# Optimization experiments

Hardware: AMD Instinct MI355X
Metric: run time of the kernel (lower is better)

The kernel has to match this reference:

```python
import jax, jax.numpy as jnp
import numpy as np

C = 256          # channels
G = 16           # dcn groups
K = 3            # dcn kernel size (P = K*K sampling points)
PAD = 1
DIL = 1
OFFSET_SCALE = 1.0
HIDDEN = 4 * C   # mlp_ratio = 4
EPS = 1e-6


def layer_norm(x, g, b):
    mu = x.mean(-1, keepdims=True)
    var = jnp.mean((x - mu) ** 2, -1, keepdims=True)
    return (x - mu) * jax.lax.rsqrt(var + EPS) * g + b


def grid_sample_bilinear(img, grid):
    """img: (B,Cg,H,W); grid: (B,L,P,2) xy in [-1,1].
    Matches F.grid_sample(mode='bilinear', padding_mode='zeros', align_corners=False)."""
    B, Cg, H, W = img.shape
    x = (grid[..., 0] + 1.0) * (W * 0.5) - 0.5
    y = (grid[..., 1] + 1.0) * (H * 0.5) - 0.5
    x0f = jnp.floor(x); y0f = jnp.floor(y)
    wx1 = x - x0f; wy1 = y - y0f
    x0 = x0f.astype(jnp.int32); y0 = y0f.astype(jnp.int32)
    flat = img.reshape(B, Cg, H * W)

    def tap(ix, iy, w):
        valid = (ix >= 0) & (ix < W) & (iy >= 0) & (iy < H)
        idx = jnp.clip(iy, 0, H - 1) * W + jnp.clip(ix, 0, W - 1)
        v = jnp.take_along_axis(flat, idx.reshape(B, 1, -1), axis=2)
        v = v.reshape(B, Cg, idx.shape[1], idx.shape[2])
        return v * (w * valid)[:, None]

    return (tap(x0, y0, (1 - wx1) * (1 - wy1))
            + tap(x0 + 1, y0, wx1 * (1 - wy1))
            + tap(x0, y0 + 1, (1 - wx1) * wy1)
            + tap(x0 + 1, y0 + 1, wx1 * wy1))


def dcnv3(x, dw_w, dw_b, off_w, off_b, mask_w, mask_b, inp_w, inp_b, out_w, out_b):
    """DCNv3 forward (dcnv3_core_pytorch math), x: (N,H,W,C) channels_last."""
    N, H, W, Cc = x.shape
    Cg = Cc // G
    P = K * K
    xp = x @ inp_w.T + inp_b                             # input_proj
    x1 = jax.lax.conv_general_dilated(
        x, dw_w, (1, 1), [(PAD, PAD), (PAD, PAD)],
        dimension_numbers=('NHWC', 'HWIO', 'NHWC'),
        feature_group_count=Cc) + dw_b                   # depthwise conv
    off = (x1 @ off_w.T + off_b).reshape(N, H, W, G, P, 2)
    m = jax.nn.softmax((x1 @ mask_w.T + mask_b).reshape(N, H, W, G, P), axis=-1)
    Hin, Win = H + 2 * PAD, W + 2 * PAD
    xpad = jnp.pad(xp, ((0, 0), (PAD, PAD), (PAD, PAD), (0, 0)))
    base = (DIL * (K - 1)) // 2
    ry = (jnp.arange(H, dtype=x.dtype) * 1.0 + base + 0.5) / Hin
    rx = (jnp.arange(W, dtype=x.dtype) * 1.0 + base + 0.5) / Win
    ref = jnp.stack([jnp.broadcast_to(rx[None, :], (H, W)),
                     jnp.broadcast_to(ry[:, None], (H, W))], -1)   # (H,W,2) xy
    xs = (jnp.arange(K, dtype=x.dtype) * DIL - base) / Win
    ys = (jnp.arange(K, dtype=x.dtype) * DIL - base) / Hin
    gx, gy = jnp.meshgrid(xs, ys, indexing='ij')         # w-major order as in torch ref
    grid = jnp.stack([gx, gy], -1).reshape(P, 2)
    norm = jnp.array([Win, Hin], dtype=x.dtype)
    loc = (ref[None, :, :, None, None, :] + grid * OFFSET_SCALE
           + off * (OFFSET_SCALE / norm))                # (N,H,W,G,P,2)
    sg = 2.0 * loc - 1.0
    img = xpad.reshape(N, Hin, Win, G, Cg).transpose(0, 3, 4, 1, 2).reshape(N * G, Cg, Hin, Win)
    sgr = sg.transpose(0, 3, 1, 2, 4, 5).reshape(N * G, H * W, P, 2)
    sampled = grid_sample_bilinear(img, sgr)             # (N*G,Cg,HW,P)
    mr = m.transpose(0, 3, 1, 2, 4).reshape(N * G, 1, H * W, P)
    out = (sampled * mr).sum(-1).reshape(N, G, Cg, H * W)
    out = out.transpose(0, 3, 1, 2).reshape(N, H, W, Cc)
    return out @ out_w.T + out_b                         # output_proj


def setup_inputs() -> dict:
    key = jax.random.key(0)
    ks = jax.random.split(key, 10)
    N, H, W = 8, 56, 56
    P = K * K

    def rn(k, shape, s):
        return jax.random.normal(k, shape, dtype=jnp.float32) * s

    return {
        'x': jax.random.normal(ks[0], (N, H, W, C), dtype=jnp.float32),
        'ln1_g': jnp.ones((C,), jnp.float32), 'ln1_b': jnp.zeros((C,), jnp.float32),
        'dw_w': rn(ks[1], (K, K, 1, C), 0.1), 'dw_b': jnp.zeros((C,), jnp.float32),
        'off_w': rn(ks[2], (G * P * 2, C), 0.02), 'off_b': jnp.zeros((G * P * 2,), jnp.float32),
        'mask_w': rn(ks[3], (G * P, C), 0.02), 'mask_b': jnp.zeros((G * P,), jnp.float32),
        'inp_w': rn(ks[4], (C, C), 0.05), 'inp_b': jnp.zeros((C,), jnp.float32),
        'out_w': rn(ks[5], (C, C), 0.05), 'out_b': jnp.zeros((C,), jnp.float32),
        'ln2_g': jnp.ones((C,), jnp.float32), 'ln2_b': jnp.zeros((C,), jnp.float32),
        'fc1_w': rn(ks[6], (HIDDEN, C), 0.05), 'fc1_b': jnp.zeros((HIDDEN,), jnp.float32),
        'fc2_w': rn(ks[7], (C, HIDDEN), 0.05), 'fc2_b': jnp.zeros((C,), jnp.float32),
    }


def reference(x, ln1_g, ln1_b, dw_w, dw_b, off_w, off_b, mask_w, mask_b,
              inp_w, inp_b, out_w, out_b, ln2_g, ln2_b, fc1_w, fc1_b, fc2_w, fc2_b):
    # pre-norm block, no layer_scale, drop_path=0
    y = x + dcnv3(layer_norm(x, ln1_g, ln1_b), dw_w, dw_b, off_w, off_b,
                  mask_w, mask_b, inp_w, inp_b, out_w, out_b)
    h = layer_norm(y, ln2_g, ln2_b)
    h = jax.nn.gelu(h @ fc1_w.T + fc1_b, approximate=False)
    return y + (h @ fc2_w.T + fc2_b)
```

## Files before the change

### kernel.cpp

```cpp
#include <hip/hip_runtime.h>
#include <hip/hip_bf16.h>
#include <math.h>

#define NTOK 25088
#define HW_  3136
#define HH   56
#define WW   56
#define CCH  256
#define NGRP 16
#define NPTS 9
#define HIDN 1024
#define NOFFM 432
#define TPB  8

typedef __attribute__((ext_vector_type(8))) __bf16 bf16x8;
typedef __attribute__((ext_vector_type(4))) __bf16 bf16x4;
typedef __attribute__((ext_vector_type(4))) float  f32x4;

static __device__ __forceinline__ void gl_lds16(const void* g, void* l) {
    __builtin_amdgcn_global_load_lds((const __attribute__((address_space(1))) void*)g,
                                     (__attribute__((address_space(3))) void*)l, 16, 0, 0);
}

static __device__ __forceinline__ float gelu_fast(float v) {
    float v2 = v * v;
    float z2 = fmaf(0.0713548163f * v, v2, 1.5957691216f * v);
    float r  = __builtin_amdgcn_rcpf(__expf(-z2) + 1.0f);
    return v * r;
}

__global__ __launch_bounds__(256)
void cvt_all_kernel(const float* __restrict__ inp_w, const float* __restrict__ out_w,
                    const float* __restrict__ off_w, const float* __restrict__ mask_w,
                    const float* __restrict__ fc1_w, const float* __restrict__ fc2_w,
                    const float* __restrict__ off_b, const float* __restrict__ mask_b,
                    __bf16* wib, __bf16* wob, __bf16* wcat, __bf16* w1b, __bf16* w2b,
                    float* bcat) {
    int i = blockIdx.x * 256 + threadIdx.x;
    if (i >= 191488) {
        int j = i - 191488;
        if (j < 432) bcat[j] = (j < 288) ? off_b[j] : mask_b[j - 288];
        return;
    }
    const float* s; __bf16* d; int off;
    if (i < 16384)       { s = inp_w;  d = wib;          off = i; }
    else if (i < 32768)  { s = out_w;  d = wob;          off = i - 16384; }
    else if (i < 51200)  { s = off_w;  d = wcat;         off = i - 32768; }
    else if (i < 60416)  { s = mask_w; d = wcat + 73728; off = i - 51200; }
    else if (i < 125952) { s = fc1_w;  d = w1b;          off = i - 60416; }
    else                 { s = fc2_w;  d = w2b;          off = i - 125952; }
    float4 v = ((const float4*)s)[off];
    bf16x4 o = {(__bf16)v.x, (__bf16)v.y, (__bf16)v.z, (__bf16)v.w};
    ((bf16x4*)d)[off] = o;
}

__global__ __launch_bounds__(256)
void ln_f_kernel(const float* __restrict__ x, const float* __restrict__ g,
                 const float* __restrict__ b, __bf16* __restrict__ outb) {
    int gid  = blockIdx.x * 256 + threadIdx.x;
    int t    = gid >> 6;
    int lane = threadIdx.x & 63;
    if (t >= NTOK) return;
    float4 v = ((const float4*)(x + (size_t)t * CCH))[lane];
    float s = v.x + v.y + v.z + v.w;
#pragma unroll
    for (int o = 1; o < 64; o <<= 1) s += __shfl_xor(s, o);
    float mu = s * 0.00390625f;
    float dx = v.x - mu, dy = v.y - mu, dz = v.z - mu, dw = v.w - mu;
    float q = dx * dx + dy * dy + dz * dz + dw * dw;
#pragma unroll
    for (int o = 1; o < 64; o <<= 1) q += __shfl_xor(q, o);
    float rstd = rsqrtf(q * 0.00390625f + 1e-6f);
    float4 gg = ((const float4*)g)[lane];
    float4 bb = ((const float4*)b)[lane];
    bf16x4 ob = {(__bf16)(dx * rstd * gg.x + bb.x), (__bf16)(dy * rstd * gg.y + bb.y),
                 (__bf16)(dz * rstd * gg.z + bb.z), (__bf16)(dw * rstd * gg.w + bb.w)};
    ((bf16x4*)(outb + (size_t)t * CCH))[lane] = ob;
}

__global__ __launch_bounds__(256)
void ln_b_kernel(const __bf16* __restrict__ x, const float* __restrict__ g,
                 const float* __restrict__ b, __bf16* __restrict__ outb) {
    int gid  = blockIdx.x * 256 + threadIdx.x;
    int t    = gid >> 6;
    int lane = threadIdx.x & 63;
    if (t >= NTOK) return;
    bf16x4 vb = ((const bf16x4*)(x + (size_t)t * CCH))[lane];
    float vx = (float)vb[0], vy = (float)vb[1], vz = (float)vb[2], vw = (float)vb[3];
    float s = vx + vy + vz + vw;
#pragma unroll
    for (int o = 1; o < 64; o <<= 1) s += __shfl_xor(s, o);
    float mu = s * 0.00390625f;
    float dx = vx - mu, dy = vy - mu, dz = vz - mu, dw = vw - mu;
    float q = dx * dx + dy * dy + dz * dz + dw * dw;
#pragma unroll
    for (int o = 1; o < 64; o <<= 1) q += __shfl_xor(q, o);
    float rstd = rsqrtf(q * 0.00390625f + 1e-6f);
    float4 gg = ((const float4*)g)[lane];
    float4 bb = ((const float4*)b)[lane];
    bf16x4 ob = {(__bf16)(dx * rstd * gg.x + bb.x), (__bf16)(dy * rstd * gg.y + bb.y),
                 (__bf16)(dz * rstd * gg.z + bb.z), (__bf16)(dw * rstd * gg.w + bb.w)};
    ((bf16x4*)(outb + (size_t)t * CCH))[lane] = ob;
}

__global__ __launch_bounds__(256)
void dwconv_kernel(const __bf16* __restrict__ ln, const float* __restrict__ wt,
                   const float* __restrict__ bias, __bf16* __restrict__ out) {
    int gid = blockIdx.x * 256 + threadIdx.x;
    int t = gid >> 6;
    int cq = gid & 63;
    if (t >= NTOK) return;
    int n = t / HW_, hw = t % HW_;
    int h = hw / WW, w0 = hw % WW;
    float4 a = ((const float4*)bias)[cq];
    const bf16x4* l4 = (const bf16x4*)ln;
    const float4* w4 = (const float4*)wt;
#pragma unroll
    for (int ky = 0; ky < 3; ++ky) {
        int y = h + ky - 1;
        if (y < 0 || y >= HH) continue;
#pragma unroll
        for (int kx = 0; kx < 3; ++kx) {
            int x = w0 + kx - 1;
            if (x < 0 || x >= WW) continue;
            bf16x4 v = l4[(size_t)(n * HW_ + y * WW + x) * 64 + cq];
            float4 ww = w4[(ky * 3 + kx) * 64 + cq];
            a.x += (float)v[0] * ww.x; a.y += (float)v[1] * ww.y;
            a.z += (float)v[2] * ww.z; a.w += (float)v[3] * ww.w;
        }
    }
    bf16x4 ob = {(__bf16)a.x, (__bf16)a.y, (__bf16)a.z, (__bf16)a.w};
    ((bf16x4*)out)[(size_t)t * 64 + cq] = ob;
}

template <int EPI>
static __device__ __forceinline__ void gemm_body(
        const __bf16* __restrict__ A, const __bf16* __restrict__ W,
        const float* __restrict__ bias, const float* __restrict__ residf,
        const __bf16* __restrict__ residb, float* __restrict__ outf,
        __bf16* __restrict__ outb, const int Ndim, const int Kdim,
        const int NB, const int lin) {
    __shared__ __align__(16) __bf16 Alds[2][64 * 32];
    __shared__ __align__(16) __bf16 Blds[2][128 * 32];

    const int tid  = threadIdx.x;
    const int w    = tid >> 6;
    const int lane = tid & 63;
    const int m0 = (lin / NB) * 64;
    const int n0 = (lin % NB) * 128;
    const int wr = (w >> 1) * 32;
    const int wc = (w & 1) * 64;

    f32x4 acc[2][4];
#pragma unroll
    for (int i = 0; i < 2; ++i)
#pragma unroll
        for (int j = 0; j < 4; ++j) acc[i][j] = (f32x4){0.f, 0.f, 0.f, 0.f};

    const int pA   = tid;
    const int arow = pA >> 2, abyte = ((pA & 3) ^ ((pA >> 4) & 3)) * 16;
    const int pB1  = tid + 256;
    const int br0  = tid >> 2, br1 = pB1 >> 2;
    int bR0 = n0 + ((br0 >> 6) << 6) + 4 * (br0 & 15) + ((br0 >> 4) & 3);
    int bR1 = n0 + ((br1 >> 6) << 6) + 4 * (br1 & 15) + ((br1 >> 4) & 3);
    if (bR0 > Ndim - 1) bR0 = Ndim - 1;
    if (bR1 > Ndim - 1) bR1 = Ndim - 1;
    const int bb0 = ((tid & 3) ^ ((tid >> 3) & 3)) * 16;
    const int bb1 = ((pB1 & 3) ^ ((pB1 >> 3) & 3)) * 16;

    const char* Ab = (const char*)A;
    const char* Wb = (const char*)W;
    char* AL = (char*)&Alds[0][0];
    char* BL = (char*)&Blds[0][0];
    const size_t rb  = (size_t)Kdim * 2;
    const size_t sA  = (size_t)(m0 + arow) * rb + abyte;
    const size_t sB0 = (size_t)bR0 * rb + bb0;
    const size_t sB1 = (size_t)bR1 * rb + bb1;
    const int dof = w * 1024;

#define STAGE(BUF, KB)                                                 \
    do {                                                               \
        gl_lds16(Ab + sA  + (KB), AL + (BUF) * 4096 + dof);            \
        gl_lds16(Wb + sB0 + (KB), BL + (BUF) * 8192 + dof);            \
        gl_lds16(Wb + sB1 + (KB), BL + (BUF) * 8192 + 4096 + dof);     \
    } while (0)

    const int mrow = lane & 15;
    const int q    = lane >> 4;
    const int kA   = ((q ^ (mrow >> 2)) & 3) * 16;
    const int kB   = ((q ^ (mrow >> 1)) & 3) * 16;

    int cur = 0;
    STAGE(0, 0);
    __syncthreads();
    for (int k0 = 0; k0 < Kdim; k0 += 32) {
        const bool more = (k0 + 32 < Kdim);
        if (more) STAGE(cur ^ 1, (size_t)(k0 + 32) * 2);
        bf16x8 af[2], bfr[4];
#pragma unroll
        for (int i = 0; i < 2; ++i)
            af[i] = *(const bf16x8*)(AL + cur * 4096 + (wr + i * 16 + mrow) * 64 + kA);
#pragma unroll
        for (int i = 0; i < 4; ++i)
            bfr[i] = *(const bf16x8*)(BL + cur * 8192 + (wc + i * 16 + mrow) * 64 + kB);
#pragma unroll
        for (int mi = 0; mi < 2; ++mi)
#pragma unroll
            for (int ni = 0; ni < 4; ++ni)
                acc[mi][ni] = __builtin_amdgcn_mfma_f32_16x16x32_bf16(af[mi], bfr[ni], acc[mi][ni], 0, 0, 0);
        if (more) {
            __syncthreads();
            cur ^= 1;
        }
    }
#undef STAGE

    const int coll = lane & 15;
    const int rowh = (lane >> 4) * 4;
    const int col0 = n0 + wc + 4 * coll;
    if (col0 < Ndim) {
        const float4 bv = *(const float4*)(bias + col0);
#pragma unroll
        for (int mi = 0; mi < 2; ++mi) {
#pragma unroll
            for (int j = 0; j < 4; ++j) {
                const int row = m0 + wr + mi * 16 + rowh + j;
                const size_t idx = (size_t)row * (size_t)Ndim + col0;
                float4 v = make_float4(acc[mi][0][j] + bv.x, acc[mi][1][j] + bv.y,
                                       acc[mi][2][j] + bv.z, acc[mi][3][j] + bv.w);
                if (EPI == 2) {
                    bf16x4 ob = {(__bf16)gelu_fast(v.x), (__bf16)gelu_fast(v.y),
                                 (__bf16)gelu_fast(v.z), (__bf16)gelu_fast(v.w)};
                    *(bf16x4*)(outb + idx) = ob;
                } else if (EPI == 3) {
                    bf16x4 ob = {(__bf16)v.x, (__bf16)v.y, (__bf16)v.z, (__bf16)v.w};
                    *(bf16x4*)(outb + idx) = ob;
                } else if (EPI == 4) {
                    const float4 r = *(const float4*)(residf + idx);
                    bf16x4 ob = {(__bf16)(v.x + r.x), (__bf16)(v.y + r.y),
                                 (__bf16)(v.z + r.z), (__bf16)(v.w + r.w)};
                    *(bf16x4*)(outb + idx) = ob;
                } else {
                    const bf16x4 r = *(const bf16x4*)(residb + idx);
                    v.x += (float)r[0]; v.y += (float)r[1];
                    v.z += (float)r[2]; v.w += (float)r[3];
                    *(float4*)(outf + idx) = v;
                }
            }
        }
    }
}

template <int EPI>
__global__ __launch_bounds__(256, 6)
void gemm_kernel(const __bf16* __restrict__ A, const __bf16* __restrict__ W,
                 const float* __restrict__ bias, const float* __restrict__ residf,
                 const __bf16* __restrict__ residb, float* __restrict__ outf,
                 __bf16* __restrict__ outb, const int Ndim, const int Kdim, const int NB) {
    const int chunk = gridDim.x >> 3;
    const int lin   = (blockIdx.x & 7) * chunk + (blockIdx.x >> 3);
    gemm_body<EPI>(A, W, bias, residf, residb, outf, outb, Ndim, Kdim, NB, lin);
}

__global__ __launch_bounds__(256, 6)
void gemm_dual_kernel(const __bf16* __restrict__ A1, const __bf16* __restrict__ W1,
                      const float* __restrict__ b1, __bf16* __restrict__ o1,
                      const int N1, const int NB1, const int split,
                      const __bf16* __restrict__ A2, const __bf16* __restrict__ W2,
                      const float* __restrict__ b2, __bf16* __restrict__ o2,
                      const int N2, const int NB2) {
    const int chunk = gridDim.x >> 3;
    const int lin   = (blockIdx.x & 7) * chunk + (blockIdx.x >> 3);
    if (lin < split)
        gemm_body<3>(A1, W1, b1, nullptr, nullptr, nullptr, o1, N1, 256, NB1, lin);
    else
        gemm_body<3>(A2, W2, b2, nullptr, nullptr, nullptr, o2, N2, 256, NB2, lin - split);
}

__global__ __launch_bounds__(256)
void dcn_kernel(const __bf16* __restrict__ xp, const __bf16* __restrict__ om,
                __bf16* __restrict__ out) {
    __shared__ __align__(16) __bf16 rawb[TPB][NOFFM];
    __shared__ ushort4 sidx[NPTS][TPB * NGRP];
    __shared__ float4  swt[NPTS][TPB * NGRP];
    const int tid = threadIdx.x;
    const int bid = blockIdx.x;
    const int b   = (bid & 7) * 392 + (bid >> 3);
    const int t0  = b * TPB;

    for (int e = tid; e < (TPB * NOFFM) / 8; e += 256)
        *(bf16x8*)(&rawb[0][0] + e * 8) = *(const bf16x8*)(om + (size_t)t0 * NOFFM + e * 8);
    __syncthreads();

    if (tid < TPB * NGRP) {
        const int lt = tid >> 4, g = tid & 15;
        __bf16* m = &rawb[lt][288 + g * 9];
        float e[9];
        float mx = -1e30f;
#pragma unroll
        for (int p = 0; p < 9; ++p) { e[p] = (float)m[p]; mx = fmaxf(mx, e[p]); }
        float s = 0.f;
#pragma unroll
        for (int p = 0; p < 9; ++p) { e[p] = __expf(e[p] - mx); s += e[p]; }
        const float inv = 1.f / s;
#pragma unroll
        for (int p = 0; p < 9; ++p) m[p] = (__bf16)(e[p] * inv);
    }
    __syncthreads();

    for (int e = tid; e < TPB * NGRP * NPTS; e += 256) {
        const int lt = e / 144, r = e % 144, g = r / 9, p = r % 9;
        const int t  = t0 + lt;
        const int hw = t % HW_;
        const int h = hw / WW, w0 = hw % WW;
        const float offx = (float)rawb[lt][g * 18 + p * 2 + 0];
        const float offy = (float)rawb[lt][g * 18 + p * 2 + 1];
        const float pm   = (float)rawb[lt][288 + g * 9 + p];
        const int kx = p / 3, ky = p % 3;
        const float fx = (float)(w0 + kx - 1) + offx;
        const float fy = (float)(h  + ky - 1) + offy;
        const float x0f = floorf(fx), y0f = floorf(fy);
        const float wx = fx - x0f, wy = fy - y0f;
        const int x0 = (int)x0f, y0 = (int)y0f;
        const bool xv0 = (unsigned)x0 < WW, xv1 = (unsigned)(x0 + 1) < WW;
        const bool yv0 = (unsigned)y0 < HH, yv1 = (unsigned)(y0 + 1) < HH;
        const int xc0 = min(max(x0, 0), WW - 1), xc1 = min(max(x0 + 1, 0), WW - 1);
        const int yc0 = min(max(y0, 0), HH - 1), yc1 = min(max(y0 + 1, 0), HH - 1);
        const int tg = lt * 16 + g;
        sidx[p][tg] = make_ushort4((unsigned short)(yc0 * WW + xc0),
                                   (unsigned short)(yc0 * WW + xc1),
                                   (unsigned short)(yc1 * WW + xc0),
                                   (unsigned short)(yc1 * WW + xc1));
        swt[p][tg]  = make_float4((xv0 && yv0) ? (1.f - wx) * (1.f - wy) * pm : 0.f,
                                  (xv1 && yv0) ? wx * (1.f - wy) * pm : 0.f,
                                  (xv0 && yv1) ? (1.f - wx) * wy * pm : 0.f,
                                  (xv1 && yv1) ? wx * wy * pm : 0.f);
    }
    __syncthreads();

    const int lt = tid >> 5, lane = tid & 31;
    const int g = lane >> 1;
    const int t = t0 + lt;
    const int n = t / HW_;
    const int tg = lt * 16 + g;
    const __bf16* base = xp + (size_t)n * HW_ * CCH + lane * 8;
    float acc[8] = {0.f, 0.f, 0.f, 0.f, 0.f, 0.f, 0.f, 0.f};
#pragma unroll
    for (int p = 0; p < NPTS; ++p) {
        const ushort4 id = sidx[p][tg];
        const float4  wv = swt[p][tg];
        bf16x8 v0 = *(const bf16x8*)(base + (size_t)id.x * CCH);
        bf16x8 v1 = *(const bf16x8*)(base + (size_t)id.y * CCH);
        bf16x8 v2 = *(const bf16x8*)(base + (size_t)id.z * CCH);
        bf16x8 v3 = *(const bf16x8*)(base + (size_t)id.w * CCH);
#pragma unroll
        for (int k = 0; k < 8; ++k)
            acc[k] += wv.x * (float)v0[k] + wv.y * (float)v1[k]
                    + wv.z * (float)v2[k] + wv.w * (float)v3[k];
    }
    bf16x8 ob;
#pragma unroll
    for (int k = 0; k < 8; ++k) ob[k] = (__bf16)acc[k];
    *(bf16x8*)(out + (size_t)t * CCH + lane * 8) = ob;
}

extern "C" void kernel_launch(void* const* d_in, const int* in_sizes, int n_in,
                              void* d_out, int out_size, void* d_ws, size_t ws_size,
                              hipStream_t stream) {
    const float* x      = (const float*)d_in[0];
    const float* ln1_g  = (const float*)d_in[1];
    const float* ln1_b  = (const float*)d_in[2];
    const float* dw_w   = (const float*)d_in[3];
    const float* dw_b   = (const float*)d_in[4];
    const float* off_w  = (const float*)d_in[5];
    const float* off_b  = (const float*)d_in[6];
    const float* mask_w = (const float*)d_in[7];
    const float* mask_b = (const float*)d_in[8];
    const float* inp_w  = (const float*)d_in[9];
    const float* inp_b  = (const float*)d_in[10];
    const float* out_w  = (const float*)d_in[11];
    const float* out_b  = (const float*)d_in[12];
    const float* ln2_g  = (const float*)d_in[13];
    const float* ln2_b  = (const float*)d_in[14];
    const float* fc1_w  = (const float*)d_in[15];
    const float* fc1_b  = (const float*)d_in[16];
    const float* fc2_w  = (const float*)d_in[17];
    const float* fc2_b  = (const float*)d_in[18];
    float* out = (float*)d_out;

    char* ws = (char*)d_ws;
    size_t o = 0;
    auto alloc = [&](size_t bytes) { size_t r = o; o += (bytes + 255) & ~(size_t)255; return r; };
    __bf16* yb    = (__bf16*)(ws + alloc((size_t)NTOK * CCH * 2));
    __bf16* x1b   = (__bf16*)(ws + alloc((size_t)NTOK * CCH * 2));
    __bf16* lnb   = (__bf16*)(ws + alloc((size_t)NTOK * CCH * 2));
    __bf16* xpb   = (__bf16*)(ws + alloc((size_t)NTOK * CCH * 2));
    __bf16* offmb = (__bf16*)(ws + alloc((size_t)NTOK * NOFFM * 2));
    alloc(6 * 1024 * 1024);
    __bf16* wib   = (__bf16*)(ws + alloc((size_t)65536 * 2));
    __bf16* wob   = (__bf16*)(ws + alloc((size_t)65536 * 2));
    __bf16* wcat  = (__bf16*)(ws + alloc((size_t)110592 * 2));
    __bf16* w1b   = (__bf16*)(ws + alloc((size_t)262144 * 2));
    __bf16* w2b   = (__bf16*)(ws + alloc((size_t)262144 * 2));
    float*  bcat  = (float*)(ws + alloc((size_t)432 * 4));
    if (ws_size < o) return;

    __bf16* dcnb = lnb;
    __bf16* l2b  = x1b;
    __bf16* h1b  = lnb;

    cvt_all_kernel<<<750, 256, 0, stream>>>(inp_w, out_w, off_w, mask_w, fc1_w, fc2_w,
                                            off_b, mask_b, wib, wob, wcat, w1b, w2b, bcat);

    ln_f_kernel<<<NTOK / 4, 256, 0, stream>>>(x, ln1_g, ln1_b, lnb);
    dwconv_kernel<<<NTOK / 4, 256, 0, stream>>>(lnb, dw_w, dw_b, x1b);
    gemm_dual_kernel<<<392 * 4 + 392 * 2, 256, 0, stream>>>(
        x1b, wcat, bcat, offmb, NOFFM, 4, 392 * 4,
        lnb, wib, inp_b, xpb, 256, 2);
    dcn_kernel<<<NTOK / TPB, 256, 0, stream>>>(xpb, offmb, dcnb);
    gemm_kernel<4><<<392 * 2, 256, 0, stream>>>(dcnb, wob, out_b, x, nullptr, nullptr, yb, 256, 256, 2);
    ln_b_kernel<<<NTOK / 4, 256, 0, stream>>>(yb, ln2_g, ln2_b, l2b);
    gemm_kernel<2><<<392 * 8, 256, 0, stream>>>(l2b, w1b, fc1_b, nullptr, nullptr, nullptr, h1b, 1024, 256, 8);
    gemm_kernel<5><<<392 * 2, 256, 0, stream>>>(h1b, w2b, fc2_b, nullptr, yb, out, nullptr, 256, 1024, 2);
}
```

Baseline: 171.9 us.

## Triple-stage GEMM prefetch with vmcnt waits; fp16 DCN weights and occupancy bound

The GEMM main loop now issues two tiles of async global-to-LDS loads up front. It waits on a partial vmcnt count plus raw s_barriers instead of a full __syncthreads per iteration, so the next tile's loads stay in flight during the MFMA work. The DCN kernel stores its bilinear×mask weights in shared memory as fp16 instead of fp32, which halves that LDS footprint and read traffic, and it gains a launch_bounds occupancy hint of 6. The fp16 weights slightly reduce precision, and the hand-written vmcnt counting depends on exactly three loads per stage.

```diff
diff --git a/kernel.cpp b/kernel.cpp
--- a/kernel.cpp
+++ b/kernel.cpp
@@ -16,6 +16,7 @@
 typedef __attribute__((ext_vector_type(8))) __bf16 bf16x8;
 typedef __attribute__((ext_vector_type(4))) __bf16 bf16x4;
 typedef __attribute__((ext_vector_type(4))) float  f32x4;
+typedef __attribute__((ext_vector_type(4))) _Float16 f16x4;
 
 static __device__ __forceinline__ void gl_lds16(const void* g, void* l) {
     __builtin_amdgcn_global_load_lds((const __attribute__((address_space(1))) void*)g,
@@ -178,11 +179,12 @@
     const size_t sB1 = (size_t)bR1 * rb + bb1;
     const int dof = w * 1024;
 
-#define STAGE(BUF, KB)                                                 \
-    do {                                                               \
-        gl_lds16(Ab + sA  + (KB), AL + (BUF) * 4096 + dof);            \
-        gl_lds16(Wb + sB0 + (KB), BL + (BUF) * 8192 + dof);            \
-        gl_lds16(Wb + sB1 + (KB), BL + (BUF) * 8192 + 4096 + dof);     \
+#define STAGE(BUF, TILE)                                                        \
+    do {                                                                        \
+        const size_t kb_ = (size_t)(TILE) * 64;                                 \
+        gl_lds16(Ab + sA  + kb_, AL + (BUF) * 4096 + dof);                      \
+        gl_lds16(Wb + sB0 + kb_, BL + (BUF) * 8192 + dof);                      \
+        gl_lds16(Wb + sB1 + kb_, BL + (BUF) * 8192 + 4096 + dof);               \
     } while (0)
 
     const int mrow = lane & 15;
@@ -190,28 +192,28 @@
     const int kA   = ((q ^ (mrow >> 2)) & 3) * 16;
     const int kB   = ((q ^ (mrow >> 1)) & 3) * 16;
 
-    int cur = 0;
+    const int nt = Kdim >> 5;
     STAGE(0, 0);
-    __syncthreads();
-    for (int k0 = 0; k0 < Kdim; k0 += 32) {
-        const bool more = (k0 + 32 < Kdim);
-        if (more) STAGE(cur ^ 1, (size_t)(k0 + 32) * 2);
+    if (nt > 1) STAGE(1, 1);
+    for (int i = 0; i < nt; ++i) {
+        const int cur = i & 1;
+        if (i + 1 < nt) asm volatile("s_waitcnt vmcnt(3)" ::: "memory");
+        else            asm volatile("s_waitcnt vmcnt(0)" ::: "memory");
+        __builtin_amdgcn_s_barrier();
         bf16x8 af[2], bfr[4];
 #pragma unroll
-        for (int i = 0; i < 2; ++i)
-            af[i] = *(const bf16x8*)(AL + cur * 4096 + (wr + i * 16 + mrow) * 64 + kA);
-#pragma unroll
-        for (int i = 0; i < 4; ++i)
-            bfr[i] = *(const bf16x8*)(BL + cur * 8192 + (wc + i * 16 + mrow) * 64 + kB);
+        for (int ii = 0; ii < 2; ++ii)
+            af[ii] = *(const bf16x8*)(AL + cur * 4096 + (wr + ii * 16 + mrow) * 64 + kA);
+#pragma unroll
+        for (int ii = 0; ii < 4; ++ii)
+            bfr[ii] = *(const bf16x8*)(BL + cur * 8192 + (wc + ii * 16 + mrow) * 64 + kB);
 #pragma unroll
         for (int mi = 0; mi < 2; ++mi)
 #pragma unroll
             for (int ni = 0; ni < 4; ++ni)
                 acc[mi][ni] = __builtin_amdgcn_mfma_f32_16x16x32_bf16(af[mi], bfr[ni], acc[mi][ni], 0, 0, 0);
-        if (more) {
-            __syncthreads();
-            cur ^= 1;
-        }
+        __builtin_amdgcn_s_barrier();
+        if (i + 2 < nt) STAGE(cur, i + 2);
     }
 #undef STAGE
 
@@ -277,12 +279,12 @@
         gemm_body<3>(A2, W2, b2, nullptr, nullptr, nullptr, o2, N2, 256, NB2, lin - split);
 }
 
-__global__ __launch_bounds__(256)
+__global__ __launch_bounds__(256, 6)
 void dcn_kernel(const __bf16* __restrict__ xp, const __bf16* __restrict__ om,
                 __bf16* __restrict__ out) {
     __shared__ __align__(16) __bf16 rawb[TPB][NOFFM];
     __shared__ ushort4 sidx[NPTS][TPB * NGRP];
-    __shared__ float4  swt[NPTS][TPB * NGRP];
+    __shared__ f16x4   swt[NPTS][TPB * NGRP];
     const int tid = threadIdx.x;
     const int bid = blockIdx.x;
     const int b   = (bid & 7) * 392 + (bid >> 3);
@@ -331,10 +333,12 @@
                                    (unsigned short)(yc0 * WW + xc1),
                                    (unsigned short)(yc1 * WW + xc0),
                                    (unsigned short)(yc1 * WW + xc1));
-        swt[p][tg]  = make_float4((xv0 && yv0) ? (1.f - wx) * (1.f - wy) * pm : 0.f,
-                                  (xv1 && yv0) ? wx * (1.f - wy) * pm : 0.f,
-                                  (xv0 && yv1) ? (1.f - wx) * wy * pm : 0.f,
-                                  (xv1 && yv1) ? wx * wy * pm : 0.f);
+        f16x4 wv;
+        wv[0] = (_Float16)((xv0 && yv0) ? (1.f - wx) * (1.f - wy) * pm : 0.f);
+        wv[1] = (_Float16)((xv1 && yv0) ? wx * (1.f - wy) * pm : 0.f);
+        wv[2] = (_Float16)((xv0 && yv1) ? (1.f - wx) * wy * pm : 0.f);
+        wv[3] = (_Float16)((xv1 && yv1) ? wx * wy * pm : 0.f);
+        swt[p][tg] = wv;
     }
     __syncthreads();
 
@@ -348,15 +352,17 @@
 #pragma unroll
     for (int p = 0; p < NPTS; ++p) {
         const ushort4 id = sidx[p][tg];
-        const float4  wv = swt[p][tg];
+        const f16x4   wh = swt[p][tg];
+        const float wx = (float)wh[0], wy = (float)wh[1];
+        const float wz = (float)wh[2], ww = (float)wh[3];
         bf16x8 v0 = *(const bf16x8*)(base + (size_t)id.x * CCH);
         bf16x8 v1 = *(const bf16x8*)(base + (size_t)id.y * CCH);
         bf16x8 v2 = *(const bf16x8*)(base + (size_t)id.z * CCH);
         bf16x8 v3 = *(const bf16x8*)(base + (size_t)id.w * CCH);
 #pragma unroll
         for (int k = 0; k < 8; ++k)
-            acc[k] += wv.x * (float)v0[k] + wv.y * (float)v1[k]
-                    + wv.z * (float)v2[k] + wv.w * (float)v3[k];
+            acc[k] += wx * (float)v0[k] + wy * (float)v1[k]
+                    + wz * (float)v2[k] + ww * (float)v3[k];
     }
     bf16x8 ob;
 #pragma unroll
```

Result: slower. 540.5 us (+214.5%).
